# Kernel tuning notes

Hardware: AMD Instinct MI355X
Metric: run time of the kernel (lower is better)

The kernel has to match this reference:

```python
import jax, jax.numpy as jnp
import numpy as np

N_VIEWS = 3
N = 20000            # samples per omic view
NT = N_VIEWS * N     # homogeneous node count
E = 800000           # number of edges
R = 6                # num_relations
B = 4                # num_bases
H = 1                # heads
D = 128              # proj_dim == hidden_channels
IN_FEAT = 2000
NUM_LABELS = 5
NEG_SLOPE = 0.2      # PyG leaky_relu default slope


def setup_inputs() -> dict:
    key = jax.random.key(0)
    ks = jax.random.split(key, 16)
    inp = {}
    for i in range(N_VIEWS):
        inp[f"x{i}"] = jax.random.normal(ks[i], (N, IN_FEAT), jnp.float32)
        inp[f"w_proj{i}"] = jax.random.normal(ks[3 + i], (IN_FEAT, D), jnp.float32) / np.sqrt(IN_FEAT)
        inp[f"b_proj{i}"] = jnp.zeros((D,), jnp.float32)
    inp["edge_src"] = jax.random.randint(ks[6], (E,), 0, NT, jnp.int32)
    inp["edge_dst"] = jax.random.randint(ks[7], (E,), 0, NT, jnp.int32)
    inp["edge_type"] = jax.random.randint(ks[8], (E,), 0, R, jnp.int32)
    inp["basis"] = jax.random.normal(ks[9], (B, D, H * D), jnp.float32) / np.sqrt(D)
    inp["comp"] = jax.random.normal(ks[10], (R, B), jnp.float32) / np.sqrt(B)
    inp["att_q"] = jax.random.normal(ks[11], (H * D, H), jnp.float32) / np.sqrt(D)
    inp["att_k"] = jax.random.normal(ks[12], (H * D, H), jnp.float32) / np.sqrt(D)
    inp["conv_bias"] = jnp.zeros((H * D,), jnp.float32)
    inp["w_int"] = jax.random.normal(ks[13], (N_VIEWS * H * D, NUM_LABELS), jnp.float32) / np.sqrt(N_VIEWS * D)
    inp["b_int"] = jnp.zeros((NUM_LABELS,), jnp.float32)
    return inp


def rgat_conv(x, edge_src, edge_dst, edge_type, basis, comp, att_q, att_k, bias):
    """PyG RGATConv: basis-decomposed relational transform + additive
    across-relation self-attention (dim=1), sum aggregation, concat heads."""
    e = edge_src.shape[0]
    # relation weights from bases: [R, D, H*D]
    w = jnp.einsum('rb,bio->rio', comp, basis)
    # transform every node under every relation: [R, NT, H*D]
    xw = jnp.einsum('nd,rdo->rno', x, w)
    xi = xw[edge_type, edge_dst]   # [E, H*D] transformed target feats
    xj = xw[edge_type, edge_src]   # [E, H*D] transformed source feats
    q = xi @ att_q                 # [E, H]
    k = xj @ att_k                 # [E, H]
    alpha = jax.nn.leaky_relu(q + k, NEG_SLOPE)
    # softmax over incoming edges of each target node (across relations)
    amax = jax.lax.stop_gradient(jax.ops.segment_max(alpha, edge_dst, num_segments=NT))
    ealpha = jnp.exp(alpha - amax[edge_dst])
    denom = jax.ops.segment_sum(ealpha, edge_dst, num_segments=NT)
    alpha = ealpha / (denom[edge_dst] + 1e-16)
    msg = (xj.reshape(e, H, D) * alpha[:, :, None]).reshape(e, H * D)
    out = jax.ops.segment_sum(msg, edge_dst, num_segments=NT)  # [NT, H*D]
    return out + bias


def reference(x0, x1, x2, w_proj0, b_proj0, w_proj1, b_proj1, w_proj2, b_proj2,
              edge_src, edge_dst, edge_type, basis, comp, att_q, att_k,
              conv_bias, w_int, b_int):
    # per-omic projection + relu, then concat to homogeneous node matrix
    h = jnp.concatenate([
        jax.nn.relu(x0 @ w_proj0 + b_proj0),
        jax.nn.relu(x1 @ w_proj1 + b_proj1),
        jax.nn.relu(x2 @ w_proj2 + b_proj2),
    ], axis=0)                                        # [NT, D]
    h = jax.nn.relu(rgat_conv(h, edge_src, edge_dst, edge_type,
                              basis, comp, att_q, att_k, conv_bias))
    # node-type gather: nodes are ordered by type in the homogeneous graph
    views = h.reshape(N_VIEWS, N, H * D)              # [V, N, D]
    feat = jnp.transpose(views, (1, 0, 2)).reshape(N, N_VIEWS * H * D)
    # LinearIntegration: concat views -> linear to classes
    return feat @ w_int + b_int                        # [N, NUM_LABELS]
```

## Files before the change

kernel.cpp:

```cpp
#include <hip/hip_runtime.h>

#define NV 3
#define NN 20000
#define NTT 60000
#define NE 800000
#define NR 6
#define NB 4
#define DD 128
#define INF 2000
#define NL 5
#define LDT 40

typedef __attribute__((ext_vector_type(8))) short short8;
typedef __attribute__((ext_vector_type(4))) float f32x4;

__device__ __forceinline__ unsigned short f2bf(float f) {
    unsigned int u = __float_as_uint(f);
    u += 0x7FFFu + ((u >> 16) & 1u);
    return (unsigned short)(u >> 16);
}
__device__ __forceinline__ float bf2f(unsigned short h) {
    return __uint_as_float(((unsigned int)h) << 16);
}


__global__ void prep_wT(const float* __restrict__ w0, const float* __restrict__ w1,
                        const float* __restrict__ w2, unsigned short* __restrict__ wT) {
    int idx = blockIdx.x * 256 + threadIdx.x;
    if (idx >= NV * DD * INF) return;
    int v = idx / (DD * INF);
    int rem = idx - v * DD * INF;
    int n = rem / INF;
    int k = rem - n * INF;
    const float* w = (v == 0) ? w0 : ((v == 1) ? w1 : w2);
    wT[idx] = f2bf(w[(size_t)k * DD + n]);
}

__global__ void prep_wrel(const float* __restrict__ basis, const float* __restrict__ comp,
                          unsigned short* __restrict__ wTrel) {
    int idx = blockIdx.x * 256 + threadIdx.x;
    if (idx >= NR * DD * DD) return;
    int r = idx / (DD * DD);
    int rem = idx - r * DD * DD;
    int o = rem / DD;
    int d = rem - o * DD;
    float s = 0.f;
    #pragma unroll
    for (int b = 0; b < NB; b++) s += comp[r * NB + b] * basis[((size_t)b * DD + d) * DD + o];
    wTrel[idx] = f2bf(s);
}

__global__ void prep_qkvec(const float* __restrict__ basis, const float* __restrict__ comp,
                           const float* __restrict__ att_q, const float* __restrict__ att_k,
                           float* __restrict__ qvec, float* __restrict__ kvec) {
    int idx = blockIdx.x * 256 + threadIdx.x;
    if (idx >= 2 * NR * DD) return;
    int sel = idx / (NR * DD);
    int rem = idx - sel * (NR * DD);
    int r = rem / DD;
    int d = rem - r * DD;
    const float* att = sel ? att_k : att_q;
    float s = 0.f;
    #pragma unroll
    for (int b = 0; b < NB; b++) {
        float cb = comp[r * NB + b];
        float t = 0.f;
        for (int o = 0; o < DD; o++) t += basis[((size_t)b * DD + d) * DD + o] * att[o];
        s += cb * t;
    }
    (sel ? kvec : qvec)[r * DD + d] = s;
}

__global__ void zero2(int* __restrict__ a, int* __restrict__ b) {
    int i = blockIdx.x * 256 + threadIdx.x;
    if (i < NTT) { a[i] = 0; b[i] = 0; }
}

__global__ __launch_bounds__(256) void proj_gemm(
    const float* __restrict__ x0, const float* __restrict__ x1, const float* __restrict__ x2,
    const float* __restrict__ b0, const float* __restrict__ b1, const float* __restrict__ b2,
    const unsigned short* __restrict__ wT, unsigned short* __restrict__ hout) {
    __shared__ unsigned short lds_a[128 * LDT];
    __shared__ unsigned short lds_b[128 * LDT];
    int v = blockIdx.y;
    const float* x = (v == 0) ? x0 : ((v == 1) ? x1 : x2);
    const float* bias = (v == 0) ? b0 : ((v == 1) ? b1 : b2);
    const unsigned short* wTv = wT + (size_t)v * DD * INF;

    int t = threadIdx.x;
    int sr = t >> 1, sh = t & 1;
    int gr = blockIdx.x * 128 + sr;
    int lane = t & 63, wid = t >> 6;
    int wm = wid >> 1, wn = wid & 1;
    int lm = lane & 15, lq = lane >> 4;

    f32x4 acc[4][4];
    #pragma unroll
    for (int i = 0; i < 4; i++)
        #pragma unroll
        for (int j = 0; j < 4; j++) {
            acc[i][j][0] = 0.f; acc[i][j][1] = 0.f; acc[i][j][2] = 0.f; acc[i][j][3] = 0.f;
        }

    const int KT = (INF + 31) / 32;
    for (int kk = 0; kk < KT; kk++) {
        int k0 = kk * 32 + sh * 16;
        if (kk < KT - 1 && gr < NN) {
            const float4* src = (const float4*)(x + (size_t)gr * INF + k0);
            #pragma unroll
            for (int j = 0; j < 4; j++) {
                float4 f = src[j];
                ushort4 u;
                u.x = f2bf(f.x); u.y = f2bf(f.y); u.z = f2bf(f.z); u.w = f2bf(f.w);
                *(ushort4*)&lds_a[sr * LDT + sh * 16 + j * 4] = u;
            }
        } else {
            for (int j = 0; j < 16; j++) {
                int k = k0 + j;
                float f = (gr < NN && k < INF) ? x[(size_t)gr * INF + k] : 0.f;
                lds_a[sr * LDT + sh * 16 + j] = f2bf(f);
            }
        }
        if (kk < KT - 1) {
            const uint4* src = (const uint4*)(wTv + (size_t)sr * INF + k0);
            *(uint4*)&lds_b[sr * LDT + sh * 16] = src[0];
            *(uint4*)&lds_b[sr * LDT + sh * 16 + 8] = src[1];
        } else {
            for (int j = 0; j < 16; j++) {
                int k = k0 + j;
                lds_b[sr * LDT + sh * 16 + j] = (k < INF) ? wTv[(size_t)sr * INF + k] : (unsigned short)0;
            }
        }
        __syncthreads();
        short8 af[4], bfr[4];
        #pragma unroll
        for (int i = 0; i < 4; i++)
            af[i] = *(const short8*)&lds_a[(wm * 64 + i * 16 + lm) * LDT + lq * 8];
        #pragma unroll
        for (int j = 0; j < 4; j++)
            bfr[j] = *(const short8*)&lds_b[(wn * 64 + j * 16 + lm) * LDT + lq * 8];
        #pragma unroll
        for (int i = 0; i < 4; i++)
            #pragma unroll
            for (int j = 0; j < 4; j++)
                acc[i][j] = __builtin_amdgcn_mfma_f32_16x16x32_bf16(af[i], bfr[j], acc[i][j], 0, 0, 0);
        __syncthreads();
    }
    #pragma unroll
    for (int i = 0; i < 4; i++) {
        int lr = wm * 64 + i * 16 + lq * 4;
        #pragma unroll
        for (int j = 0; j < 4; j++) {
            int c = wn * 64 + j * 16 + lm;
            float bv = bias[c];
            #pragma unroll
            for (int u = 0; u < 4; u++) {
                int grow = blockIdx.x * 128 + lr + u;
                if (grow < NN) {
                    float o = acc[i][j][u] + bv;
                    o = fmaxf(o, 0.f);
                    hout[((size_t)(v * NN + grow)) * DD + c] = f2bf(o);
                }
            }
        }
    }
}

__global__ __launch_bounds__(256) void xw_gemm(
    const unsigned short* __restrict__ h, const unsigned short* __restrict__ wTrel,
    unsigned short* __restrict__ xw) {
    __shared__ unsigned short lds_a[128 * LDT];
    __shared__ unsigned short lds_b[128 * LDT];
    int r = blockIdx.y;
    const unsigned short* wTr = wTrel + (size_t)r * DD * DD;
    int t = threadIdx.x;
    int sr = t >> 1, sh = t & 1;
    int grow = blockIdx.x * 128 + sr;
    int grc = (grow < NTT) ? grow : (NTT - 1);
    int lane = t & 63, wid = t >> 6;
    int wm = wid >> 1, wn = wid & 1;
    int lm = lane & 15, lq = lane >> 4;

    f32x4 acc[4][4];
    #pragma unroll
    for (int i = 0; i < 4; i++)
        #pragma unroll
        for (int j = 0; j < 4; j++) {
            acc[i][j][0] = 0.f; acc[i][j][1] = 0.f; acc[i][j][2] = 0.f; acc[i][j][3] = 0.f;
        }

    #pragma unroll
    for (int kk = 0; kk < 4; kk++) {
        int k0 = kk * 32 + sh * 16;
        const uint4* asrc = (const uint4*)(h + (size_t)grc * DD + k0);
        *(uint4*)&lds_a[sr * LDT + sh * 16] = asrc[0];
        *(uint4*)&lds_a[sr * LDT + sh * 16 + 8] = asrc[1];
        const uint4* bsrc = (const uint4*)(wTr + (size_t)sr * DD + k0);
        *(uint4*)&lds_b[sr * LDT + sh * 16] = bsrc[0];
        *(uint4*)&lds_b[sr * LDT + sh * 16 + 8] = bsrc[1];
        __syncthreads();
        short8 af[4], bfr[4];
        #pragma unroll
        for (int i = 0; i < 4; i++)
            af[i] = *(const short8*)&lds_a[(wm * 64 + i * 16 + lm) * LDT + lq * 8];
        #pragma unroll
        for (int j = 0; j < 4; j++)
            bfr[j] = *(const short8*)&lds_b[(wn * 64 + j * 16 + lm) * LDT + lq * 8];
        #pragma unroll
        for (int i = 0; i < 4; i++)
            #pragma unroll
            for (int j = 0; j < 4; j++)
                acc[i][j] = __builtin_amdgcn_mfma_f32_16x16x32_bf16(af[i], bfr[j], acc[i][j], 0, 0, 0);
        __syncthreads();
    }
    #pragma unroll
    for (int i = 0; i < 4; i++) {
        int lr = wm * 64 + i * 16 + lq * 4;
        #pragma unroll
        for (int j = 0; j < 4; j++) {
            int c = wn * 64 + j * 16 + lm;
            #pragma unroll
            for (int u = 0; u < 4; u++) {
                int g2 = blockIdx.x * 128 + lr + u;
                if (g2 < NTT)
                    xw[((size_t)r * NTT + g2) * DD + c] = f2bf(acc[i][j][u]);
            }
        }
    }
}

__global__ void qk_nodes(const unsigned short* __restrict__ h, const float* __restrict__ qvec,
                         const float* __restrict__ kvec, float* __restrict__ qn,
                         float* __restrict__ kn) {
    int wid = threadIdx.x >> 6, lane = threadIdx.x & 63;
    int node = blockIdx.x * 4 + wid;
    if (node >= NTT) return;
    unsigned int u = *(const unsigned int*)(h + (size_t)node * DD + lane * 2);
    float h0 = bf2f(u & 0xffff), h1 = bf2f(u >> 16);
    #pragma unroll
    for (int r = 0; r < NR; r++) {
        float pq = h0 * qvec[r * DD + lane * 2] + h1 * qvec[r * DD + lane * 2 + 1];
        float pk = h0 * kvec[r * DD + lane * 2] + h1 * kvec[r * DD + lane * 2 + 1];
        #pragma unroll
        for (int off = 32; off; off >>= 1) {
            pq += __shfl_xor(pq, off);
            pk += __shfl_xor(pk, off);
        }
        if (lane == 0) {
            qn[r * NTT + node] = pq;
            kn[r * NTT + node] = pk;
        }
    }
}

__global__ void hist(const int* __restrict__ dst, int* __restrict__ indeg) {
    int e = blockIdx.x * 256 + threadIdx.x;
    if (e < NE) atomicAdd(&indeg[dst[e]], 1);
}

__global__ __launch_bounds__(1024) void scan_indeg(const int* __restrict__ indeg,
                                                   int* __restrict__ start) {
    int t = threadIdx.x;
    const int per = (NTT + 1023) / 1024;
    int base = t * per;
    int s = 0;
    for (int i = 0; i < per; i++) {
        int idx = base + i;
        if (idx < NTT) s += indeg[idx];
    }
    int lane = t & 63, wid = t >> 6;
    __shared__ int wsum[16];
    int v = s;
    #pragma unroll
    for (int off = 1; off < 64; off <<= 1) {
        int u = __shfl_up(v, off);
        if (lane >= off) v += u;
    }
    if (lane == 63) wsum[wid] = v;
    __syncthreads();
    if (t < 16) {
        int w = wsum[t];
        #pragma unroll
        for (int off = 1; off < 16; off <<= 1) {
            int u = __shfl_up(w, off);
            if (t >= off) w += u;
        }
        wsum[t] = w;
    }
    __syncthreads();
    int excl = (v - s) + (wid ? wsum[wid - 1] : 0);
    int run = excl;
    for (int i = 0; i < per; i++) {
        int idx = base + i;
        if (idx < NTT) {
            start[idx] = run;
            run += indeg[idx];
        }
    }
    if (t == 1023) start[NTT] = run;
}

__global__ void scatter(const int* __restrict__ dst, const int* __restrict__ start,
                        int* __restrict__ cursor, int* __restrict__ elist) {
    int e = blockIdx.x * 256 + threadIdx.x;
    if (e < NE) {
        int d = dst[e];
        int pos = atomicAdd(&cursor[d], 1);
        elist[start[d] + pos] = e;
    }
}

__global__ void aggregate(const int* __restrict__ elist, const int* __restrict__ start,
                          const int* __restrict__ etype, const int* __restrict__ esrc,
                          const float* __restrict__ qn, const float* __restrict__ kn,
                          const unsigned short* __restrict__ xw,
                          const float* __restrict__ conv_bias, float* __restrict__ h2) {
    int wid = threadIdx.x >> 6, lane = threadIdx.x & 63;
    int node = blockIdx.x * 4 + wid;
    if (node >= NTT) return;
    int s0 = start[node], s1 = start[node + 1];
    float a0 = 0.f, a1 = 0.f, denom = 0.f;
    for (int i = s0; i < s1; i++) {
        int e = elist[i];
        int tt = etype[e], ss = esrc[e];
        float al = qn[tt * NTT + node] + kn[tt * NTT + ss];
        al = (al > 0.f) ? al : 0.2f * al;
        float w = __expf(al);
        denom += w;
        unsigned int u = *(const unsigned int*)(xw + ((size_t)tt * NTT + ss) * DD + lane * 2);
        a0 += w * bf2f(u & 0xffff);
        a1 += w * bf2f(u >> 16);
    }
    float rdenom = 1.f / (denom + 1e-16f);
    float o0 = fmaxf(a0 * rdenom + conv_bias[lane * 2], 0.f);
    float o1 = fmaxf(a1 * rdenom + conv_bias[lane * 2 + 1], 0.f);
    float2 o;
    o.x = o0;
    o.y = o1;
    *(float2*)&h2[(size_t)node * DD + lane * 2] = o;
}

__global__ void final_linear(const float* __restrict__ h2, const float* __restrict__ w_int,
                             const float* __restrict__ b_int, float* __restrict__ out) {
    int wid = threadIdx.x >> 6, lane = threadIdx.x & 63;
    int node = blockIdx.x * 4 + wid;
    if (node >= NN) return;
    float acc[NL] = {0.f, 0.f, 0.f, 0.f, 0.f};
    for (int j = lane; j < NV * DD; j += 64) {
        int v = j >> 7, d = j & 127;
        float f = h2[((size_t)(v * NN + node)) * DD + d];
        #pragma unroll
        for (int c = 0; c < NL; c++) acc[c] += f * w_int[j * NL + c];
    }
    #pragma unroll
    for (int c = 0; c < NL; c++) {
        float s = acc[c];
        #pragma unroll
        for (int off = 32; off; off >>= 1) s += __shfl_xor(s, off);
        if (lane == 0) out[(size_t)node * NL + c] = s + b_int[c];
    }
}

extern "C" void kernel_launch(void* const* d_in, const int* in_sizes, int n_in, void* d_out,
                              int out_size, void* d_ws, size_t ws_size, hipStream_t stream) {
    (void)in_sizes; (void)n_in; (void)out_size; (void)ws_size;
    const float* x0 = (const float*)d_in[0];
    const float* w0 = (const float*)d_in[1];
    const float* b0 = (const float*)d_in[2];
    const float* x1 = (const float*)d_in[3];
    const float* w1 = (const float*)d_in[4];
    const float* b1 = (const float*)d_in[5];
    const float* x2 = (const float*)d_in[6];
    const float* w2 = (const float*)d_in[7];
    const float* b2 = (const float*)d_in[8];
    const int* esrc = (const int*)d_in[9];
    const int* edst = (const int*)d_in[10];
    const int* etype = (const int*)d_in[11];
    const float* basis = (const float*)d_in[12];
    const float* comp = (const float*)d_in[13];
    const float* att_q = (const float*)d_in[14];
    const float* att_k = (const float*)d_in[15];
    const float* conv_bias = (const float*)d_in[16];
    const float* w_int = (const float*)d_in[17];
    const float* b_int = (const float*)d_in[18];

    char* ws = (char*)d_ws;
    size_t off = 0;
    auto alloc = [&](size_t bytes) -> void* {
        void* p = ws + off;
        off += bytes;
        off = (off + 255) & ~(size_t)255;
        return p;
    };
    unsigned short* h = (unsigned short*)alloc((size_t)NTT * DD * 2);
    unsigned short* xw = (unsigned short*)alloc((size_t)NR * NTT * DD * 2);
    float* qn = (float*)alloc((size_t)NR * NTT * 4);
    float* kn = (float*)alloc((size_t)NR * NTT * 4);
    unsigned short* wT = (unsigned short*)alloc((size_t)NV * DD * INF * 2);
    unsigned short* wTrel = (unsigned short*)alloc((size_t)NR * DD * DD * 2);
    float* qvec = (float*)alloc((size_t)NR * DD * 4);
    float* kvec = (float*)alloc((size_t)NR * DD * 4);
    int* indeg = (int*)alloc((size_t)NTT * 4);
    int* cursor = (int*)alloc((size_t)NTT * 4);
    int* startp = (int*)alloc((size_t)(NTT + 1) * 4);
    int* elist = (int*)alloc((size_t)NE * 4);
    float* h2 = (float*)alloc((size_t)NTT * DD * 4);

    prep_wT<<<(NV * DD * INF + 255) / 256, 256, 0, stream>>>(w0, w1, w2, wT);
    prep_wrel<<<(NR * DD * DD + 255) / 256, 256, 0, stream>>>(basis, comp, wTrel);
    prep_qkvec<<<(2 * NR * DD + 255) / 256, 256, 0, stream>>>(basis, comp, att_q, att_k, qvec, kvec);
    zero2<<<(NTT + 255) / 256, 256, 0, stream>>>(indeg, cursor);

    proj_gemm<<<dim3((NN + 127) / 128, NV), 256, 0, stream>>>(x0, x1, x2, b0, b1, b2, wT, h);
    qk_nodes<<<(NTT + 3) / 4, 256, 0, stream>>>(h, qvec, kvec, qn, kn);
    xw_gemm<<<dim3((NTT + 127) / 128, NR), 256, 0, stream>>>(h, wTrel, xw);

    hist<<<(NE + 255) / 256, 256, 0, stream>>>(edst, indeg);
    scan_indeg<<<1, 1024, 0, stream>>>(indeg, startp);
    scatter<<<(NE + 255) / 256, 256, 0, stream>>>(edst, startp, cursor, elist);

    aggregate<<<(NTT + 3) / 4, 256, 0, stream>>>(elist, startp, etype, esrc, qn, kn, xw,
                                                 conv_bias, h2);
    final_linear<<<(NN + 3) / 4, 256, 0, stream>>>(h2, w_int, b_int, (float*)d_out);
}
```

Baseline: 936.7 us.

## Precompute edge weights in scatter and prefetch tiles in projection GEMM

The projection GEMM moves to 64-row tiles and loads the next K tile into registers while the MFMAs for the current tile run, which gives more blocks and hides global load latency. The scatter kernel now computes each edge's attention weight and writes a packed (src, type) word plus the weight in CSR order. The aggregate kernel then reads these coalesced per wavefront, broadcasts them with shuffles, and reduces the denominator across lanes, so the per-edge dependent gathers and redundant exp work are gone. In exchange, packing src into 16 bits assumes node indices below 65536, which holds for 60000 nodes, and the scatter pass writes one extra array.

```diff
diff --git a/kernel.cpp b/kernel.cpp
--- a/kernel.cpp
+++ b/kernel.cpp
@@ -80,7 +80,7 @@
     const float* __restrict__ x0, const float* __restrict__ x1, const float* __restrict__ x2,
     const float* __restrict__ b0, const float* __restrict__ b1, const float* __restrict__ b2,
     const unsigned short* __restrict__ wT, unsigned short* __restrict__ hout) {
-    __shared__ unsigned short lds_a[128 * LDT];
+    __shared__ unsigned short lds_a[64 * LDT];
     __shared__ unsigned short lds_b[128 * LDT];
     int v = blockIdx.y;
     const float* x = (v == 0) ? x0 : ((v == 1) ? x1 : x2);
@@ -88,77 +88,86 @@
     const unsigned short* wTv = wT + (size_t)v * DD * INF;
 
     int t = threadIdx.x;
-    int sr = t >> 1, sh = t & 1;
-    int gr = blockIdx.x * 128 + sr;
+    int arow = t >> 2, aq = t & 3;
+    int gr = blockIdx.x * 64 + arow;
+    bool arowok = gr < NN;
+    int brow = t >> 1, bh = t & 1;
+
     int lane = t & 63, wid = t >> 6;
     int wm = wid >> 1, wn = wid & 1;
     int lm = lane & 15, lq = lane >> 4;
 
-    f32x4 acc[4][4];
-    #pragma unroll
-    for (int i = 0; i < 4; i++)
+    f32x4 acc[2][4];
+    #pragma unroll
+    for (int i = 0; i < 2; i++)
         #pragma unroll
         for (int j = 0; j < 4; j++) {
             acc[i][j][0] = 0.f; acc[i][j][1] = 0.f; acc[i][j][2] = 0.f; acc[i][j][3] = 0.f;
         }
 
     const int KT = (INF + 31) / 32;
+    float4 fa0, fa1;
+    uint4 fb0, fb1;
+
+    auto loadA = [&](int kk) {
+        int kb = kk * 32 + aq * 8;
+        fa0 = make_float4(0.f, 0.f, 0.f, 0.f);
+        fa1 = fa0;
+        if (arowok && kb < INF) {
+            const float4* p = (const float4*)(x + (size_t)gr * INF + kb);
+            fa0 = p[0]; fa1 = p[1];
+        }
+    };
+    auto loadB = [&](int kk) {
+        int kb = kk * 32 + bh * 16;
+        fb0 = make_uint4(0, 0, 0, 0);
+        fb1 = fb0;
+        if (kb < INF) {
+            const uint4* p = (const uint4*)(wTv + (size_t)brow * INF + kb);
+            fb0 = p[0]; fb1 = p[1];
+        }
+    };
+    auto stage = [&]() {
+        ushort4 u0, u1;
+        u0.x = f2bf(fa0.x); u0.y = f2bf(fa0.y); u0.z = f2bf(fa0.z); u0.w = f2bf(fa0.w);
+        u1.x = f2bf(fa1.x); u1.y = f2bf(fa1.y); u1.z = f2bf(fa1.z); u1.w = f2bf(fa1.w);
+        *(ushort4*)&lds_a[arow * LDT + aq * 8] = u0;
+        *(ushort4*)&lds_a[arow * LDT + aq * 8 + 4] = u1;
+        *(uint4*)&lds_b[brow * LDT + bh * 16] = fb0;
+        *(uint4*)&lds_b[brow * LDT + bh * 16 + 8] = fb1;
+    };
+
+    loadA(0); loadB(0);
     for (int kk = 0; kk < KT; kk++) {
-        int k0 = kk * 32 + sh * 16;
-        if (kk < KT - 1 && gr < NN) {
-            const float4* src = (const float4*)(x + (size_t)gr * INF + k0);
-            #pragma unroll
-            for (int j = 0; j < 4; j++) {
-                float4 f = src[j];
-                ushort4 u;
-                u.x = f2bf(f.x); u.y = f2bf(f.y); u.z = f2bf(f.z); u.w = f2bf(f.w);
-                *(ushort4*)&lds_a[sr * LDT + sh * 16 + j * 4] = u;
-            }
-        } else {
-            for (int j = 0; j < 16; j++) {
-                int k = k0 + j;
-                float f = (gr < NN && k < INF) ? x[(size_t)gr * INF + k] : 0.f;
-                lds_a[sr * LDT + sh * 16 + j] = f2bf(f);
-            }
-        }
-        if (kk < KT - 1) {
-            const uint4* src = (const uint4*)(wTv + (size_t)sr * INF + k0);
-            *(uint4*)&lds_b[sr * LDT + sh * 16] = src[0];
-            *(uint4*)&lds_b[sr * LDT + sh * 16 + 8] = src[1];
-        } else {
-            for (int j = 0; j < 16; j++) {
-                int k = k0 + j;
-                lds_b[sr * LDT + sh * 16 + j] = (k < INF) ? wTv[(size_t)sr * INF + k] : (unsigned short)0;
-            }
-        }
+        stage();
         __syncthreads();
-        short8 af[4], bfr[4];
-        #pragma unroll
-        for (int i = 0; i < 4; i++)
-            af[i] = *(const short8*)&lds_a[(wm * 64 + i * 16 + lm) * LDT + lq * 8];
+        if (kk + 1 < KT) { loadA(kk + 1); loadB(kk + 1); }
+        short8 af[2], bfr[4];
+        #pragma unroll
+        for (int i = 0; i < 2; i++)
+            af[i] = *(const short8*)&lds_a[(wm * 32 + i * 16 + lm) * LDT + lq * 8];
         #pragma unroll
         for (int j = 0; j < 4; j++)
             bfr[j] = *(const short8*)&lds_b[(wn * 64 + j * 16 + lm) * LDT + lq * 8];
         #pragma unroll
-        for (int i = 0; i < 4; i++)
+        for (int i = 0; i < 2; i++)
             #pragma unroll
             for (int j = 0; j < 4; j++)
                 acc[i][j] = __builtin_amdgcn_mfma_f32_16x16x32_bf16(af[i], bfr[j], acc[i][j], 0, 0, 0);
         __syncthreads();
     }
     #pragma unroll
-    for (int i = 0; i < 4; i++) {
-        int lr = wm * 64 + i * 16 + lq * 4;
+    for (int i = 0; i < 2; i++) {
+        int lr = wm * 32 + i * 16 + lq * 4;
         #pragma unroll
         for (int j = 0; j < 4; j++) {
             int c = wn * 64 + j * 16 + lm;
             float bv = bias[c];
             #pragma unroll
             for (int u = 0; u < 4; u++) {
-                int grow = blockIdx.x * 128 + lr + u;
+                int grow = blockIdx.x * 64 + lr + u;
                 if (grow < NN) {
-                    float o = acc[i][j][u] + bv;
-                    o = fmaxf(o, 0.f);
+                    float o = fmaxf(acc[i][j][u] + bv, 0.f);
                     hout[((size_t)(v * NN + grow)) * DD + c] = f2bf(o);
                 }
             }
@@ -300,43 +309,56 @@
     if (t == 1023) start[NTT] = run;
 }
 
-__global__ void scatter(const int* __restrict__ dst, const int* __restrict__ start,
-                        int* __restrict__ cursor, int* __restrict__ elist) {
+__global__ void scatter2(const int* __restrict__ dst, const int* __restrict__ src,
+                         const int* __restrict__ typ, const int* __restrict__ start,
+                         int* __restrict__ cursor, const float* __restrict__ qn,
+                         const float* __restrict__ kn, unsigned int* __restrict__ packed,
+                         float* __restrict__ wl) {
     int e = blockIdx.x * 256 + threadIdx.x;
-    if (e < NE) {
-        int d = dst[e];
-        int pos = atomicAdd(&cursor[d], 1);
-        elist[start[d] + pos] = e;
-    }
-}
-
-__global__ void aggregate(const int* __restrict__ elist, const int* __restrict__ start,
-                          const int* __restrict__ etype, const int* __restrict__ esrc,
-                          const float* __restrict__ qn, const float* __restrict__ kn,
-                          const unsigned short* __restrict__ xw,
+    if (e >= NE) return;
+    int d = dst[e], ss = src[e], tt = typ[e];
+    float al = qn[tt * NTT + d] + kn[tt * NTT + ss];
+    al = (al > 0.f) ? al : 0.2f * al;
+    float w = __expf(al);
+    int pos = atomicAdd(&cursor[d], 1);
+    int idx = start[d] + pos;
+    packed[idx] = (unsigned)ss | ((unsigned)tt << 16);
+    wl[idx] = w;
+}
+
+__global__ void aggregate(const unsigned int* __restrict__ packed, const float* __restrict__ wl,
+                          const int* __restrict__ start, const unsigned short* __restrict__ xw,
                           const float* __restrict__ conv_bias, float* __restrict__ h2) {
     int wid = threadIdx.x >> 6, lane = threadIdx.x & 63;
     int node = blockIdx.x * 4 + wid;
     if (node >= NTT) return;
     int s0 = start[node], s1 = start[node + 1];
     float a0 = 0.f, a1 = 0.f, denom = 0.f;
-    for (int i = s0; i < s1; i++) {
-        int e = elist[i];
-        int tt = etype[e], ss = esrc[e];
-        float al = qn[tt * NTT + node] + kn[tt * NTT + ss];
-        al = (al > 0.f) ? al : 0.2f * al;
-        float w = __expf(al);
-        denom += w;
-        unsigned int u = *(const unsigned int*)(xw + ((size_t)tt * NTT + ss) * DD + lane * 2);
-        a0 += w * bf2f(u & 0xffff);
-        a1 += w * bf2f(u >> 16);
-    }
+    for (int base = s0; base < s1; base += 64) {
+        int cnt = min(64, s1 - base);
+        unsigned pk = 0;
+        float wv = 0.f;
+        if (lane < cnt) {
+            pk = packed[base + lane];
+            wv = wl[base + lane];
+        }
+        denom += wv;
+        for (int i = 0; i < cnt; i++) {
+            unsigned sp = __shfl(pk, i);
+            float sw = __shfl(wv, i);
+            unsigned ss = sp & 0xFFFFu;
+            unsigned tt = sp >> 16;
+            unsigned u = *(const unsigned int*)(xw + ((size_t)tt * NTT + ss) * DD + lane * 2);
+            a0 += sw * bf2f(u & 0xffff);
+            a1 += sw * bf2f(u >> 16);
+        }
+    }
+    #pragma unroll
+    for (int off = 32; off; off >>= 1) denom += __shfl_xor(denom, off);
     float rdenom = 1.f / (denom + 1e-16f);
-    float o0 = fmaxf(a0 * rdenom + conv_bias[lane * 2], 0.f);
-    float o1 = fmaxf(a1 * rdenom + conv_bias[lane * 2 + 1], 0.f);
     float2 o;
-    o.x = o0;
-    o.y = o1;
+    o.x = fmaxf(a0 * rdenom + conv_bias[lane * 2], 0.f);
+    o.y = fmaxf(a1 * rdenom + conv_bias[lane * 2 + 1], 0.f);
     *(float2*)&h2[(size_t)node * DD + lane * 2] = o;
 }
 
@@ -403,7 +425,8 @@
     int* indeg = (int*)alloc((size_t)NTT * 4);
     int* cursor = (int*)alloc((size_t)NTT * 4);
     int* startp = (int*)alloc((size_t)(NTT + 1) * 4);
-    int* elist = (int*)alloc((size_t)NE * 4);
+    unsigned int* packed = (unsigned int*)alloc((size_t)NE * 4);
+    float* wl = (float*)alloc((size_t)NE * 4);
     float* h2 = (float*)alloc((size_t)NTT * DD * 4);
 
     prep_wT<<<(NV * DD * INF + 255) / 256, 256, 0, stream>>>(w0, w1, w2, wT);
@@ -411,15 +434,15 @@
     prep_qkvec<<<(2 * NR * DD + 255) / 256, 256, 0, stream>>>(basis, comp, att_q, att_k, qvec, kvec);
     zero2<<<(NTT + 255) / 256, 256, 0, stream>>>(indeg, cursor);
 
-    proj_gemm<<<dim3((NN + 127) / 128, NV), 256, 0, stream>>>(x0, x1, x2, b0, b1, b2, wT, h);
+    proj_gemm<<<dim3((NN + 63) / 64, NV), 256, 0, stream>>>(x0, x1, x2, b0, b1, b2, wT, h);
     qk_nodes<<<(NTT + 3) / 4, 256, 0, stream>>>(h, qvec, kvec, qn, kn);
     xw_gemm<<<dim3((NTT + 127) / 128, NR), 256, 0, stream>>>(h, wTrel, xw);
 
     hist<<<(NE + 255) / 256, 256, 0, stream>>>(edst, indeg);
     scan_indeg<<<1, 1024, 0, stream>>>(indeg, startp);
-    scatter<<<(NE + 255) / 256, 256, 0, stream>>>(edst, startp, cursor, elist);
-
-    aggregate<<<(NTT + 3) / 4, 256, 0, stream>>>(elist, startp, etype, esrc, qn, kn, xw,
-                                                 conv_bias, h2);
+    scatter2<<<(NE + 255) / 256, 256, 0, stream>>>(edst, esrc, etype, startp, cursor, qn, kn,
+                                                   packed, wl);
+
+    aggregate<<<(NTT + 3) / 4, 256, 0, stream>>>(packed, wl, startp, xw, conv_bias, h2);
     final_linear<<<(NN + 3) / 4, 256, 0, stream>>>(h2, w_int, b_int, (float*)d_out);
 }
```

Result: faster. 899.5 us (-4.0%).
